# Kernel optimization log

Measured on AMD Instinct MI355X. Metric: run time of the kernel, lower is better.

Reference implementation:

```python
import jax, jax.numpy as jnp
import numpy as np

B, S, D, H = 4, 2048, 1024, 16
HD = D // H

def setup_inputs() -> dict:
    key = jax.random.key(0)
    ks = jax.random.split(key, 9)
    sc = 0.02
    return {
        "x": jax.random.normal(ks[0], (B, S, D), dtype=jnp.float32),
        "Wq": jax.random.normal(ks[1], (D, D), dtype=jnp.float32) * sc,
        "bq": jax.random.normal(ks[2], (D,), dtype=jnp.float32) * sc,
        "Wk": jax.random.normal(ks[3], (D, D), dtype=jnp.float32) * sc,
        "bk": jax.random.normal(ks[4], (D,), dtype=jnp.float32) * sc,
        "Wv": jax.random.normal(ks[5], (D, D), dtype=jnp.float32) * sc,
        "bv": jax.random.normal(ks[6], (D,), dtype=jnp.float32) * sc,
        "Wo": jax.random.normal(ks[7], (D, D), dtype=jnp.float32) * sc,
        "bo": jax.random.normal(ks[8], (D,), dtype=jnp.float32) * sc,
    }

def reference(x, Wq, bq, Wk, bk, Wv, bv, Wo, bo):
    b, n, d = x.shape
    # projections, split heads: [b, h, n, hd]
    def split_heads(t):
        return t.reshape(b, n, H, HD).transpose(0, 2, 1, 3)
    q = split_heads(x @ Wq.T + bq)
    k = split_heads(x @ Wk.T + bk)
    v = split_heads(x @ Wv.T + bv)
    # scores [b, h, n, n], causal mask (triu above diagonal -> -inf)
    scores = jnp.einsum("bhqd,bhkd->bhqk", q, k)
    causal = jnp.tril(jnp.ones((n, n), dtype=bool))  # True = keep
    scores = jnp.where(causal, scores, -jnp.inf)
    # note: module divides by sqrt(head_dim) AFTER masking, same result
    attn = jax.nn.softmax(scores / jnp.sqrt(jnp.float32(HD)), axis=-1)
    ctx = jnp.einsum("bhqk,bhkd->bhqd", attn, v)
    ctx = ctx.transpose(0, 2, 1, 3).reshape(b, n, d)
    return ctx @ Wo.T + bo
```

## Files before the change

kernel.cpp:

```cpp
#include <hip/hip_runtime.h>
#include <stdint.h>

#define BATCH 4
#define S_LEN 2048
#define D_DIM 1024
#define NH 16
#define HD 64
#define M_ROWS (BATCH * S_LEN)
#define NQB (S_LEN / 128)
#define QSCALE 0.18033688011f

using u16 = unsigned short;
typedef __attribute__((ext_vector_type(8))) __bf16 bf16x8;
typedef __attribute__((ext_vector_type(4))) float f32x4;
typedef __attribute__((ext_vector_type(16))) float f32x16;
typedef __attribute__((ext_vector_type(8))) unsigned short u16x8;

__device__ __forceinline__ float exp2fast(float x) { return __builtin_amdgcn_exp2f(x); }

__device__ __forceinline__ u16 f2bf(float f) {
  unsigned u = __builtin_bit_cast(unsigned, f);
  u += 0x7fffu + ((u >> 16) & 1u);
  return (u16)(u >> 16);
}
__device__ __forceinline__ unsigned pk2(float lo, float hi) {
  return (unsigned)f2bf(lo) | ((unsigned)f2bf(hi) << 16);
}

__global__ void cvt_bf16_kernel(const float* __restrict__ in, u16* __restrict__ out, int n4) {
  int i = blockIdx.x * blockDim.x + threadIdx.x;
  if (i < n4) {
    float4 v = ((const float4*)in)[i];
    ushort4 o;
    o.x = f2bf(v.x); o.y = f2bf(v.y); o.z = f2bf(v.z); o.w = f2bf(v.w);
    ((ushort4*)out)[i] = o;
  }
}

__global__ void cvt_w_kernel(const float* __restrict__ W0, const float* __restrict__ W1,
                             const float* __restrict__ W2, const float* __restrict__ W3,
                             u16* __restrict__ out) {
  int y = blockIdx.y;
  const float* src = (y == 0) ? W0 : (y == 1) ? W1 : (y == 2) ? W2 : W3;
  u16* dst = out + (size_t)y * D_DIM * D_DIM;
  int i = blockIdx.x * blockDim.x + threadIdx.x;
  float4 v = ((const float4*)src)[i];
  ushort4 o;
  o.x = f2bf(v.x); o.y = f2bf(v.y); o.z = f2bf(v.z); o.w = f2bf(v.w);
  ((ushort4*)dst)[i] = o;
}

__device__ __forceinline__ void stage_tile(const u16* __restrict__ src, int srcK,
                                           u16* dst, int w, int lane) {
#pragma unroll
  for (int i = 0; i < 4; ++i) {
    int ic = w * 4 + i;
    int c = ic * 64 + lane;
    int row = c >> 3, g = c & 7, gs = g ^ (row & 7);
    __builtin_amdgcn_global_load_lds(
        (const __attribute__((address_space(1))) void*)(src + (size_t)row * srcK + gs * 8),
        (__attribute__((address_space(3))) void*)(dst + ic * 512), 16, 0, 0);
  }
}

__global__ __launch_bounds__(256)
void gemm_qkv_kernel(const u16* __restrict__ A, const u16* __restrict__ Bt,
                     const float* __restrict__ bq, const float* __restrict__ bk,
                     const float* __restrict__ bv,
                     u16* __restrict__ Qo, u16* __restrict__ Ko, u16* __restrict__ Vo) {
  __shared__ __align__(16) u16 As[128 * 64];
  __shared__ __align__(16) u16 Bs[128 * 64];
  const int tid = threadIdx.x;
  const int w = tid >> 6;
  const int lane = tid & 63;
  const int l15 = lane & 15, l4 = lane >> 4;
  const int m0 = blockIdx.y * 128, n0 = blockIdx.x * 128;
  const int wr = (w >> 1) * 64, wc = (w & 1) * 64;
  const int K = D_DIM;

  f32x4 acc[4][4] = {};

  for (int k0 = 0; k0 < K; k0 += 64) {
    __syncthreads();
    stage_tile(A + (size_t)m0 * K + k0, K, As, w, lane);
    stage_tile(Bt + (size_t)n0 * K + k0, K, Bs, w, lane);
    __syncthreads();

    bf16x8 a[4][2];
#pragma unroll
    for (int mb = 0; mb < 4; ++mb) {
#pragma unroll
      for (int ks = 0; ks < 2; ++ks) {
        int row = wr + mb * 16 + l15;
        int gsw = (ks * 4 + l4) ^ (row & 7);
        a[mb][ks] = *(const bf16x8*)(As + row * 64 + gsw * 8);
      }
    }
#pragma unroll
    for (int nb = 0; nb < 4; ++nb) {
      int row = wc + nb * 16 + l15;
      int g0 = (0 + l4) ^ (row & 7);
      int g1 = (4 + l4) ^ (row & 7);
      bf16x8 b0 = *(const bf16x8*)(Bs + row * 64 + g0 * 8);
      bf16x8 b1 = *(const bf16x8*)(Bs + row * 64 + g1 * 8);
#pragma unroll
      for (int mb = 0; mb < 4; ++mb) {
        acc[mb][nb] = __builtin_amdgcn_mfma_f32_16x16x32_bf16(a[mb][0], b0, acc[mb][nb], 0, 0, 0);
        acc[mb][nb] = __builtin_amdgcn_mfma_f32_16x16x32_bf16(a[mb][1], b1, acc[mb][nb], 0, 0, 0);
      }
    }
  }

  const int which = n0 >> 10;
  const float* bias = (which == 0) ? bq : (which == 1) ? bk : bv;
  u16* dst = (which == 0) ? Qo : (which == 1) ? Ko : Vo;
  const float scale = (which == 0) ? QSCALE : 1.0f;

#pragma unroll
  for (int mb = 0; mb < 4; ++mb) {
#pragma unroll
    for (int nb = 0; nb < 4; ++nb) {
#pragma unroll
      for (int r = 0; r < 4; ++r) {
        int m = m0 + wr + mb * 16 + l4 * 4 + r;
        int n = n0 + wc + nb * 16 + l15;
        int col = n & 1023;
        float v = (acc[mb][nb][r] + bias[col]) * scale;
        int bb = m >> 11;
        int ss = m & (S_LEN - 1);
        int hh = col >> 6;
        int hd = col & (HD - 1);
        dst[(((size_t)bb * NH + hh) * S_LEN + ss) * HD + hd] = f2bf(v);
      }
    }
  }
}

__global__ __launch_bounds__(256)
void gemm_out_kernel(const u16* __restrict__ A, const u16* __restrict__ Bt,
                     const float* __restrict__ bias, float* __restrict__ Cout) {
  __shared__ __align__(16) u16 As[128 * 64];
  __shared__ __align__(16) u16 Bs[128 * 64];
  const int tid = threadIdx.x;
  const int w = tid >> 6;
  const int lane = tid & 63;
  const int l15 = lane & 15, l4 = lane >> 4;
  const int m0 = blockIdx.y * 128, n0 = blockIdx.x * 128;
  const int wr = (w >> 1) * 64, wc = (w & 1) * 64;
  const int K = D_DIM, N = D_DIM;

  f32x4 acc[4][4] = {};

  for (int k0 = 0; k0 < K; k0 += 64) {
    __syncthreads();
    stage_tile(A + (size_t)m0 * K + k0, K, As, w, lane);
    stage_tile(Bt + (size_t)n0 * K + k0, K, Bs, w, lane);
    __syncthreads();

    bf16x8 a[4][2];
#pragma unroll
    for (int mb = 0; mb < 4; ++mb) {
#pragma unroll
      for (int ks = 0; ks < 2; ++ks) {
        int row = wr + mb * 16 + l15;
        int gsw = (ks * 4 + l4) ^ (row & 7);
        a[mb][ks] = *(const bf16x8*)(As + row * 64 + gsw * 8);
      }
    }
#pragma unroll
    for (int nb = 0; nb < 4; ++nb) {
      int row = wc + nb * 16 + l15;
      int g0 = (0 + l4) ^ (row & 7);
      int g1 = (4 + l4) ^ (row & 7);
      bf16x8 b0 = *(const bf16x8*)(Bs + row * 64 + g0 * 8);
      bf16x8 b1 = *(const bf16x8*)(Bs + row * 64 + g1 * 8);
#pragma unroll
      for (int mb = 0; mb < 4; ++mb) {
        acc[mb][nb] = __builtin_amdgcn_mfma_f32_16x16x32_bf16(a[mb][0], b0, acc[mb][nb], 0, 0, 0);
        acc[mb][nb] = __builtin_amdgcn_mfma_f32_16x16x32_bf16(a[mb][1], b1, acc[mb][nb], 0, 0, 0);
      }
    }
  }

#pragma unroll
  for (int mb = 0; mb < 4; ++mb) {
#pragma unroll
    for (int nb = 0; nb < 4; ++nb) {
#pragma unroll
      for (int r = 0; r < 4; ++r) {
        int m = m0 + wr + mb * 16 + l4 * 4 + r;
        int n = n0 + wc + nb * 16 + l15;
        Cout[(size_t)m * N + n] = acc[mb][nb][r] + bias[n];
      }
    }
  }
}

__device__ __forceinline__ void stage_k(const u16* __restrict__ Kg, size_t base, int kt,
                                        u16* Kd, int w, int lane) {
#pragma unroll
  for (int i = 0; i < 2; ++i) {
    int ic = w * 2 + i;
    int c = ic * 64 + lane;
    int row = c >> 3, g = c & 7, gs = g ^ (row & 7);
    __builtin_amdgcn_global_load_lds(
        (const __attribute__((address_space(1))) void*)(Kg + base + (size_t)(kt * 64 + row) * HD + gs * 8),
        (__attribute__((address_space(3))) void*)(Kd + ic * 512), 16, 0, 0);
  }
}

__device__ __forceinline__ void pfrag(const f32x16& st, int hi, bf16x8& fa, bf16x8& fb) {
  unsigned c0 = pk2(st[0], st[1]),   c1 = pk2(st[2], st[3]);
  unsigned c2 = pk2(st[4], st[5]),   c3 = pk2(st[6], st[7]);
  unsigned c4 = pk2(st[8], st[9]),   c5 = pk2(st[10], st[11]);
  unsigned c6 = pk2(st[12], st[13]), c7 = pk2(st[14], st[15]);
  unsigned p0 = __shfl_xor(c0, 32), p1 = __shfl_xor(c1, 32);
  unsigned p2 = __shfl_xor(c2, 32), p3 = __shfl_xor(c3, 32);
  unsigned p4 = __shfl_xor(c4, 32), p5 = __shfl_xor(c5, 32);
  unsigned p6 = __shfl_xor(c6, 32), p7 = __shfl_xor(c7, 32);
  union { unsigned u[4]; bf16x8 v; } a, b;
  a.u[0] = hi ? p2 : c0; a.u[1] = hi ? p3 : c1;
  a.u[2] = hi ? c2 : p0; a.u[3] = hi ? c3 : p1;
  b.u[0] = hi ? p6 : c4; b.u[1] = hi ? p7 : c5;
  b.u[2] = hi ? c6 : p4; b.u[3] = hi ? c7 : p5;
  fa = a.v; fb = b.v;
}

__global__ __launch_bounds__(256)
void attn_kernel(const u16* __restrict__ Q, const u16* __restrict__ Kg,
                 const u16* __restrict__ Vg, u16* __restrict__ ctx) {
  __shared__ __align__(16) u16 Ks[2][64 * 64];
  __shared__ __align__(16) u16 Vt[64 * 64];

  const int tid = threadIdx.x;
  const int w = tid >> 6, lane = tid & 63;
  const int l31 = lane & 31, hi = lane >> 5;
  const int hi4 = hi * 4, hi8 = hi * 8;
  const int bh = blockIdx.y;
  const size_t base = (size_t)bh * S_LEN * HD;
  const int b = bh >> 4, h = bh & (NH - 1);

  const int vkey = tid & 63;
  const int vd0 = (tid >> 6) * 16;

#pragma unroll 1
  for (int seg = 0; seg < 2; ++seg) {
    const int qb = seg ? (NQB - 1 - blockIdx.x) : blockIdx.x;
    const int Qw = qb * 128 + w * 32;
    const int q_g = Qw + l31;

    bf16x8 qf[4];
#pragma unroll
    for (int step = 0; step < 4; ++step)
      qf[step] = *(const bf16x8*)(Q + base + (size_t)q_g * HD + step * 16 + hi8);

    f32x16 oacc0 = {}, oacc1 = {};
    float mrun = -1e30f, lrun = 0.f;

    const int nkt = 2 * qb + 2;

    stage_k(Kg, base, 0, Ks[0], w, lane);
    u16x8 vv0, vv1;
    {
      const u16* gv = Vg + base + (size_t)vkey * HD + vd0;
      vv0 = *(const u16x8*)gv;
      vv1 = *(const u16x8*)(gv + 8);
    }

    for (int kt = 0; kt < nkt; ++kt) {
      const int cur = kt & 1;
      const bool more = (kt + 1 < nkt);

#pragma unroll
      for (int j = 0; j < 8; ++j) {
        int d0 = vd0 + j;
        Vt[d0 * 64 + (((vkey >> 3) ^ ((d0 >> 2) & 7)) << 3) + (vkey & 7)] = vv0[j];
        int d1 = vd0 + 8 + j;
        Vt[d1 * 64 + (((vkey >> 3) ^ ((d1 >> 2) & 7)) << 3) + (vkey & 7)] = vv1[j];
      }
      __syncthreads();

      if (more) {
        stage_k(Kg, base, kt + 1, Ks[cur ^ 1], w, lane);
        const u16* gv = Vg + base + (size_t)((kt + 1) * 64 + vkey) * HD + vd0;
        vv0 = *(const u16x8*)gv;
        vv1 = *(const u16x8*)(gv + 8);
      }

      const u16* Kb = &Ks[cur][0];

      if (kt * 64 <= Qw + 31) {
        f32x16 st0 = {}, st1 = {};
#pragma unroll
        for (int step = 0; step < 4; ++step) {
          int r0 = l31, r1 = 32 + l31;
          bf16x8 kf0 = *(const bf16x8*)(Kb + r0 * 64 + (((step * 2 + hi) ^ (r0 & 7)) << 3));
          bf16x8 kf1 = *(const bf16x8*)(Kb + r1 * 64 + (((step * 2 + hi) ^ (r1 & 7)) << 3));
          st0 = __builtin_amdgcn_mfma_f32_32x32x16_bf16(kf0, qf[step], st0, 0, 0, 0);
          st1 = __builtin_amdgcn_mfma_f32_32x32x16_bf16(kf1, qf[step], st1, 0, 0, 0);
        }

        if (kt * 64 + 63 > Qw) {
#pragma unroll
          for (int r = 0; r < 16; ++r) {
            int key0 = kt * 64 + hi4 + (r & 3) + 8 * (r >> 2);
            if (key0 > q_g) st0[r] = -1e30f;
            if (key0 + 32 > q_g) st1[r] = -1e30f;
          }
        }

        float tm = -1e30f;
#pragma unroll
        for (int r = 0; r < 16; ++r) { tm = fmaxf(tm, st0[r]); tm = fmaxf(tm, st1[r]); }
        tm = fmaxf(tm, __shfl_xor(tm, 32));

        if (__any(tm > mrun)) {
          float mnew = fmaxf(mrun, tm);
          float rs = exp2fast(mrun - mnew);
          mrun = mnew;
          lrun *= rs;
#pragma unroll
          for (int r = 0; r < 16; ++r) {
            float rsb = __shfl(rs, (r & 3) + 8 * (r >> 2) + hi4);
            oacc0[r] *= rsb;
            oacc1[r] *= rsb;
          }
        }

        float sum = 0.f;
#pragma unroll
        for (int r = 0; r < 16; ++r) {
          st0[r] = exp2fast(st0[r] - mrun); sum += st0[r];
          st1[r] = exp2fast(st1[r] - mrun); sum += st1[r];
        }
        sum += __shfl_xor(sum, 32);
        lrun += sum;

        bf16x8 paf0, paf1, paf2, paf3;
        pfrag(st0, hi, paf0, paf1);
        pfrag(st1, hi, paf2, paf3);

#pragma unroll
        for (int ks = 0; ks < 4; ++ks) {
          bf16x8 pa = (ks == 0) ? paf0 : (ks == 1) ? paf1 : (ks == 2) ? paf2 : paf3;
          int d0 = l31;
          bf16x8 vf0 = *(const bf16x8*)(Vt + d0 * 64 + (((ks * 2 + hi) ^ ((d0 >> 2) & 7)) << 3));
          int d1 = 32 + l31;
          bf16x8 vf1 = *(const bf16x8*)(Vt + d1 * 64 + (((ks * 2 + hi) ^ ((d1 >> 2) & 7)) << 3));
          oacc0 = __builtin_amdgcn_mfma_f32_32x32x16_bf16(pa, vf0, oacc0, 0, 0, 0);
          oacc1 = __builtin_amdgcn_mfma_f32_32x32x16_bf16(pa, vf1, oacc1, 0, 0, 0);
        }
      }
      __syncthreads();
    }

#pragma unroll
    for (int r = 0; r < 16; ++r) {
      float lr = __shfl(lrun, (r & 3) + 8 * (r >> 2) + hi4);
      float inv = 1.0f / lr;
      int srow = Qw + (r & 3) + 8 * (r >> 2) + hi4;
      size_t rowbase = ((size_t)b * S_LEN + srow) * D_DIM + h * HD;
      ctx[rowbase + l31] = f2bf(oacc0[r] * inv);
      ctx[rowbase + 32 + l31] = f2bf(oacc1[r] * inv);
    }
  }
}

extern "C" void kernel_launch(void* const* d_in, const int* in_sizes, int n_in,
                              void* d_out, int out_size, void* d_ws, size_t ws_size,
                              hipStream_t stream) {
  const float* x  = (const float*)d_in[0];
  const float* Wq = (const float*)d_in[1];
  const float* bq = (const float*)d_in[2];
  const float* Wk = (const float*)d_in[3];
  const float* bk = (const float*)d_in[4];
  const float* Wv = (const float*)d_in[5];
  const float* bv = (const float*)d_in[6];
  const float* Wo = (const float*)d_in[7];
  const float* bo = (const float*)d_in[8];

  char* ws = (char*)d_ws;
  const size_t MB = 1024 * 1024;
  u16* xb     = (u16*)(ws + 0);
  u16* Wqkvb  = (u16*)(ws + 16 * MB);
  u16* Wob    = (u16*)(ws + 22 * MB);
  u16* Qb     = (u16*)(ws + 24 * MB);
  u16* Kb     = (u16*)(ws + 40 * MB);
  u16* Vb     = (u16*)(ws + 56 * MB);
  u16* ctxb   = xb;

  cvt_bf16_kernel<<<(M_ROWS * D_DIM / 4 + 255) / 256, 256, 0, stream>>>(x, xb, M_ROWS * D_DIM / 4);
  cvt_w_kernel<<<dim3(D_DIM * D_DIM / 4 / 256, 4), 256, 0, stream>>>(Wq, Wk, Wv, Wo, Wqkvb);

  gemm_qkv_kernel<<<dim3(3 * D_DIM / 128, M_ROWS / 128), 256, 0, stream>>>(
      xb, Wqkvb, bq, bk, bv, Qb, Kb, Vb);

  attn_kernel<<<dim3(NQB / 2, BATCH * NH), 256, 0, stream>>>(Qb, Kb, Vb, ctxb);

  gemm_out_kernel<<<dim3(D_DIM / 128, M_ROWS / 128), 256, 0, stream>>>(
      ctxb, Wob, bo, (float*)d_out);
}
```

Measured before the change: 200.9 us.

## Process two 64-key tiles per barrier pair and cheapen softmax reductions

The attention loop now stages two 64-key K/V tiles per iteration, using larger double-buffered LDS arrays, so the barrier pair and the prefetch are spread over 128 keys instead of 64. The row max and row sum reductions become tree reductions over 16 values instead of serial chains, which shortens dependency chains. The bf16 packing switches from round-to-nearest to truncation via a byte-perm instruction, which is cheaper but loses rounding accuracy. The cost is more LDS and registers per block, which may lower occupancy, plus some wasted tile loads near the causal diagonal.

```diff
diff --git a/kernel.cpp b/kernel.cpp
--- a/kernel.cpp
+++ b/kernel.cpp
@@ -24,7 +24,8 @@
   return (u16)(u >> 16);
 }
 __device__ __forceinline__ unsigned pk2(float lo, float hi) {
-  return (unsigned)f2bf(lo) | ((unsigned)f2bf(hi) << 16);
+  return __builtin_amdgcn_perm(__builtin_bit_cast(unsigned, hi),
+                               __builtin_bit_cast(unsigned, lo), 0x07060302u);
 }
 
 __global__ void cvt_bf16_kernel(const float* __restrict__ in, u16* __restrict__ out, int n4) {
@@ -196,7 +197,7 @@
   }
 }
 
-__device__ __forceinline__ void stage_k(const u16* __restrict__ Kg, size_t base, int kt,
+__device__ __forceinline__ void stage_k(const u16* __restrict__ Kg, size_t base, int t64,
                                         u16* Kd, int w, int lane) {
 #pragma unroll
   for (int i = 0; i < 2; ++i) {
@@ -204,7 +205,7 @@
     int c = ic * 64 + lane;
     int row = c >> 3, g = c & 7, gs = g ^ (row & 7);
     __builtin_amdgcn_global_load_lds(
-        (const __attribute__((address_space(1))) void*)(Kg + base + (size_t)(kt * 64 + row) * HD + gs * 8),
+        (const __attribute__((address_space(1))) void*)(Kg + base + (size_t)(t64 * 64 + row) * HD + gs * 8),
         (__attribute__((address_space(3))) void*)(Kd + ic * 512), 16, 0, 0);
   }
 }
@@ -229,8 +230,8 @@
 __global__ __launch_bounds__(256)
 void attn_kernel(const u16* __restrict__ Q, const u16* __restrict__ Kg,
                  const u16* __restrict__ Vg, u16* __restrict__ ctx) {
-  __shared__ __align__(16) u16 Ks[2][64 * 64];
-  __shared__ __align__(16) u16 Vt[64 * 64];
+  __shared__ __align__(16) u16 Ks[2][2][64 * 64];
+  __shared__ __align__(16) u16 Vt[2][64 * 64];
 
   const int tid = threadIdx.x;
   const int w = tid >> 6, lane = tid & 63;
@@ -257,39 +258,50 @@
     f32x16 oacc0 = {}, oacc1 = {};
     float mrun = -1e30f, lrun = 0.f;
 
-    const int nkt = 2 * qb + 2;
-
-    stage_k(Kg, base, 0, Ks[0], w, lane);
-    u16x8 vv0, vv1;
+    const int nkt2 = qb + 1;
+
+    stage_k(Kg, base, 0, Ks[0][0], w, lane);
+    stage_k(Kg, base, 1, Ks[0][1], w, lane);
+    u16x8 va0, va1, vb0, vb1;
     {
-      const u16* gv = Vg + base + (size_t)vkey * HD + vd0;
-      vv0 = *(const u16x8*)gv;
-      vv1 = *(const u16x8*)(gv + 8);
-    }
-
-    for (int kt = 0; kt < nkt; ++kt) {
-      const int cur = kt & 1;
-      const bool more = (kt + 1 < nkt);
+      const u16* gva = Vg + base + (size_t)vkey * HD + vd0;
+      const u16* gvb = Vg + base + (size_t)(64 + vkey) * HD + vd0;
+      va0 = *(const u16x8*)gva; va1 = *(const u16x8*)(gva + 8);
+      vb0 = *(const u16x8*)gvb; vb1 = *(const u16x8*)(gvb + 8);
+    }
+
+    for (int kt2 = 0; kt2 < nkt2; ++kt2) {
+      const int cur = kt2 & 1;
+      const bool more = (kt2 + 1 < nkt2);
 
 #pragma unroll
       for (int j = 0; j < 8; ++j) {
-        int d0 = vd0 + j;
-        Vt[d0 * 64 + (((vkey >> 3) ^ ((d0 >> 2) & 7)) << 3) + (vkey & 7)] = vv0[j];
-        int d1 = vd0 + 8 + j;
-        Vt[d1 * 64 + (((vkey >> 3) ^ ((d1 >> 2) & 7)) << 3) + (vkey & 7)] = vv1[j];
+        int d0 = vd0 + j, d1 = vd0 + 8 + j;
+        int s0 = (((vkey >> 3) ^ ((d0 >> 2) & 7)) << 3) + (vkey & 7);
+        int s1 = (((vkey >> 3) ^ ((d1 >> 2) & 7)) << 3) + (vkey & 7);
+        Vt[0][d0 * 64 + s0] = va0[j];
+        Vt[0][d1 * 64 + s1] = va1[j];
+        Vt[1][d0 * 64 + s0] = vb0[j];
+        Vt[1][d1 * 64 + s1] = vb1[j];
       }
       __syncthreads();
 
       if (more) {
-        stage_k(Kg, base, kt + 1, Ks[cur ^ 1], w, lane);
-        const u16* gv = Vg + base + (size_t)((kt + 1) * 64 + vkey) * HD + vd0;
-        vv0 = *(const u16x8*)gv;
-        vv1 = *(const u16x8*)(gv + 8);
-      }
-
-      const u16* Kb = &Ks[cur][0];
-
-      if (kt * 64 <= Qw + 31) {
+        stage_k(Kg, base, 2 * (kt2 + 1), Ks[cur ^ 1][0], w, lane);
+        stage_k(Kg, base, 2 * (kt2 + 1) + 1, Ks[cur ^ 1][1], w, lane);
+        const u16* gva = Vg + base + (size_t)((kt2 + 1) * 128 + vkey) * HD + vd0;
+        const u16* gvb = Vg + base + (size_t)((kt2 + 1) * 128 + 64 + vkey) * HD + vd0;
+        va0 = *(const u16x8*)gva; va1 = *(const u16x8*)(gva + 8);
+        vb0 = *(const u16x8*)gvb; vb1 = *(const u16x8*)(gvb + 8);
+      }
+
+#pragma unroll
+      for (int hh2 = 0; hh2 < 2; ++hh2) {
+        const int kb64 = kt2 * 128 + hh2 * 64;
+        if (kb64 > Qw + 31) continue;
+        const u16* Kb = &Ks[cur][hh2][0];
+        const u16* Vb = &Vt[hh2][0];
+
         f32x16 st0 = {}, st1 = {};
 #pragma unroll
         for (int step = 0; step < 4; ++step) {
@@ -300,19 +312,24 @@
           st1 = __builtin_amdgcn_mfma_f32_32x32x16_bf16(kf1, qf[step], st1, 0, 0, 0);
         }
 
-        if (kt * 64 + 63 > Qw) {
+        if (kb64 + 63 > Qw) {
 #pragma unroll
           for (int r = 0; r < 16; ++r) {
-            int key0 = kt * 64 + hi4 + (r & 3) + 8 * (r >> 2);
+            int key0 = kb64 + hi4 + (r & 3) + 8 * (r >> 2);
             if (key0 > q_g) st0[r] = -1e30f;
             if (key0 + 32 > q_g) st1[r] = -1e30f;
           }
         }
 
-        float tm = -1e30f;
-#pragma unroll
-        for (int r = 0; r < 16; ++r) { tm = fmaxf(tm, st0[r]); tm = fmaxf(tm, st1[r]); }
-        tm = fmaxf(tm, __shfl_xor(tm, 32));
+        float mt[16];
+#pragma unroll
+        for (int r = 0; r < 16; ++r) mt[r] = fmaxf(st0[r], st1[r]);
+#pragma unroll
+        for (int s = 8; s >= 1; s >>= 1)
+#pragma unroll
+          for (int r = 0; r < 8; ++r)
+            if (r < s) mt[r] = fmaxf(mt[r], mt[r + s]);
+        float tm = fmaxf(mt[0], __shfl_xor(mt[0], 32));
 
         if (__any(tm > mrun)) {
           float mnew = fmaxf(mrun, tm);
@@ -327,14 +344,19 @@
           }
         }
 
-        float sum = 0.f;
+        float sa[16];
 #pragma unroll
         for (int r = 0; r < 16; ++r) {
-          st0[r] = exp2fast(st0[r] - mrun); sum += st0[r];
-          st1[r] = exp2fast(st1[r] - mrun); sum += st1[r];
+          st0[r] = exp2fast(st0[r] - mrun);
+          st1[r] = exp2fast(st1[r] - mrun);
+          sa[r] = st0[r] + st1[r];
         }
-        sum += __shfl_xor(sum, 32);
-        lrun += sum;
+#pragma unroll
+        for (int s = 8; s >= 1; s >>= 1)
+#pragma unroll
+          for (int r = 0; r < 8; ++r)
+            if (r < s) sa[r] += sa[r + s];
+        lrun += sa[0] + __shfl_xor(sa[0], 32);
 
         bf16x8 paf0, paf1, paf2, paf3;
         pfrag(st0, hi, paf0, paf1);
@@ -344,9 +366,9 @@
         for (int ks = 0; ks < 4; ++ks) {
           bf16x8 pa = (ks == 0) ? paf0 : (ks == 1) ? paf1 : (ks == 2) ? paf2 : paf3;
           int d0 = l31;
-          bf16x8 vf0 = *(const bf16x8*)(Vt + d0 * 64 + (((ks * 2 + hi) ^ ((d0 >> 2) & 7)) << 3));
+          bf16x8 vf0 = *(const bf16x8*)(Vb + d0 * 64 + (((ks * 2 + hi) ^ ((d0 >> 2) & 7)) << 3));
           int d1 = 32 + l31;
-          bf16x8 vf1 = *(const bf16x8*)(Vt + d1 * 64 + (((ks * 2 + hi) ^ ((d1 >> 2) & 7)) << 3));
+          bf16x8 vf1 = *(const bf16x8*)(Vb + d1 * 64 + (((ks * 2 + hi) ^ ((d1 >> 2) & 7)) << 3));
           oacc0 = __builtin_amdgcn_mfma_f32_32x32x16_bf16(pa, vf0, oacc0, 0, 0, 0);
           oacc1 = __builtin_amdgcn_mfma_f32_32x32x16_bf16(pa, vf1, oacc1, 0, 0, 0);
         }
```

Result: slower. 241.0 us (+20.0%).
